# Kernel tuning notes

Measured on AMD Instinct MI355X. Metric: run time of the kernel, lower is better.

The kernel has to match this reference:

```python
import jax, jax.numpy as jnp
import numpy as np

B, H, V, A, NANN, DEPTH = 32, 256, 512, 3, 8, 7


def preorder_perm(arity, depth):
    # level-order node index -> pre-order position permutation for a full arity-ary tree
    starts = np.cumsum([0] + [arity ** l for l in range(depth + 1)])
    order = []
    def rec(l, p):
        order.append(int(starts[l] + p))
        if l < depth:
            for c in range(arity):
                rec(l + 1, p * arity + c)
    rec(0, 0)
    return np.asarray(order, dtype=np.int32)


def setup_inputs() -> dict:
    key = jax.random.key(0)
    ks = jax.random.split(key, 12)
    s = 0.05
    return {
        "root_hiddens": jax.random.normal(ks[0], (B, H), jnp.float32),
        "ann_table": jax.random.normal(ks[1], (NANN, H), jnp.float32),
        "w1": jax.random.normal(ks[2], (2 * H, H), jnp.float32) * s,
        "b1": jnp.zeros((2 * H,), jnp.float32),
        "w2": jax.random.normal(ks[3], (V, 2 * H), jnp.float32) * s,
        "b2": jnp.zeros((V,), jnp.float32),
        "gru_w_ih": jax.random.normal(ks[4], (A, 3 * H, H), jnp.float32) * s,
        "gru_w_hh": jax.random.normal(ks[5], (A, 3 * H, H), jnp.float32) * s,
        "gru_b_ih": jnp.zeros((A, 3 * H), jnp.float32),
        "gru_b_hh": jnp.zeros((A, 3 * H), jnp.float32),
        "ann_ids": jax.random.randint(ks[6], (B,), 0, NANN, jnp.int32),
        "depth": DEPTH,
    }


def _forward(root_hiddens, ann_table, w1, b1, w2, b2,
             gru_w_ih, gru_w_hh, gru_b_ih, gru_b_hh, ann_ids, depth):
    b, h = root_hiddens.shape
    arity = gru_w_ih.shape[0]
    x = ann_table[ann_ids]                                   # [B,H] annotation embedding (GRU input at every node)
    # input-side gates are constant across the whole tree: precompute once
    gx = jnp.einsum('bh,agh->bag', x, gru_w_ih) + gru_b_ih   # [B,A,3H]
    xr, xz, xn = jnp.split(gx, 3, axis=-1)                   # each [B,A,H]

    hid = root_hiddens[:, None, :]                           # [B,1,H]
    levels = [hid]
    for _ in range(depth):
        gh = jnp.einsum('bnh,agh->bnag', hid, gru_w_hh) + gru_b_hh  # [B,n,A,3H]
        hr, hz, hn = jnp.split(gh, 3, axis=-1)
        r = jax.nn.sigmoid(xr[:, None] + hr)
        z = jax.nn.sigmoid(xz[:, None] + hz)
        n = jnp.tanh(xn[:, None] + r * hn)
        new_h = (1.0 - z) * n + z * hid[:, :, None, :]       # [B,n,A,H]
        hid = new_h.reshape(b, -1, h)                        # child c of node p -> p*A+c
        levels.append(hid)

    all_h = jnp.concatenate(levels, axis=1)                  # [B,N,H] level-order
    mid = jax.nn.sigmoid(jnp.einsum('bnh,oh->bno', all_h, w1) + b1)
    prod = jnp.einsum('bno,vo->bnv', mid, w2) + b2           # [B,N,V]
    perm = jnp.asarray(preorder_perm(arity, depth))
    return jnp.transpose(prod[:, perm, :], (1, 0, 2))        # [N,B,V] (seq-first, like pad_sequence)


def reference(root_hiddens, ann_table, w1, b1, w2, b2,
              gru_w_ih, gru_w_hh, gru_b_ih, gru_b_hh, ann_ids, depth):
    return _forward(root_hiddens, ann_table, w1, b1, w2, b2,
                    gru_w_ih, gru_w_hh, gru_b_ih, gru_b_hh, ann_ids, depth)
```

## Files before the change

### kernel.cpp

```cpp
#include <hip/hip_runtime.h>
#include <hip/hip_bf16.h>
#include <stdint.h>
#include <stddef.h>

#define NB 32
#define NH 256
#define NMID 512
#define NV 512
#define NA 3
#define NDEPTH 7
#define NNODES 3280
#define NG 2304
#define MROWS (NNODES * NB)
#define HM 64

typedef __attribute__((ext_vector_type(8))) short bf16x8;
typedef __attribute__((ext_vector_type(4))) float f32x4;

__device__ __forceinline__ unsigned short f2bf(float x) {
    union { float f; unsigned u; } v; v.f = x;
    unsigned r = v.u + 0x7fffu + ((v.u >> 16) & 1u);
    return (unsigned short)(r >> 16);
}
__device__ __forceinline__ unsigned cvt_pk_bf16(float a, float b) {
    unsigned r;
    asm("v_cvt_pk_bf16_f32 %0, %1, %2" : "=v"(r) : "v"(a), "v"(b));
    return r;
}
__device__ __forceinline__ float bf2f(unsigned short u) {
    union { unsigned u; float f; } v; v.u = ((unsigned)u) << 16;
    return v.f;
}
__device__ __forceinline__ float sigm(float x) { return 1.0f / (1.0f + __expf(-x)); }
__device__ __forceinline__ float tanh_(float x) {
    x = fminf(fmaxf(x, -15.0f), 15.0f);
    float e = __expf(2.0f * x);
    return (e - 1.0f) / (e + 1.0f);
}
__device__ __forceinline__ f32x4 splat4(float s) { f32x4 v = {s, s, s, s}; return v; }

__device__ __forceinline__ int preorder_pos(int n) {
    int start = 0, cnt = 1, l = 0;
    while (n >= start + cnt) { start += cnt; cnt *= 3; l++; }
    int p = n - start;
    int pw = 1;
    for (int j = 0; j < l - 1; j++) pw *= 3;
    int pos = 0;
    for (int k = 1; k <= l; k++) {
        int d = (p / pw) % 3;
        int e = NDEPTH - k + 1;
        int p3 = 1; for (int j = 0; j < e; j++) p3 *= 3;
        pos += 1 + d * ((p3 - 1) / 2);
        pw /= 3;
    }
    return pos;
}

__global__ void prep_all(const float* __restrict__ root, const float* __restrict__ ann_table,
                         const int* __restrict__ ann_ids,
                         const float* __restrict__ w_ih, const float* __restrict__ b_ih,
                         const float* __restrict__ whh_f, const float* __restrict__ w1_f,
                         const float* __restrict__ w2_f,
                         unsigned short* __restrict__ whh_b, unsigned short* __restrict__ w1_b,
                         unsigned short* __restrict__ w2_b,
                         float* __restrict__ gx_t, int* __restrict__ posmap,
                         unsigned short* __restrict__ hid_b) {
    int gtid = blockIdx.x * blockDim.x + threadIdx.x;
    int nth = gridDim.x * blockDim.x;
    const int n_whh = NG * NH, n_w1 = NMID * NH, n_w2 = NV * NMID;
    const int total = n_whh + n_w1 + n_w2;
    for (int i = gtid; i < total; i += nth) {
        if (i < n_whh) whh_b[i] = f2bf(whh_f[i]);
        else if (i < n_whh + n_w1) w1_b[i - n_whh] = f2bf(w1_f[i - n_whh]);
        else w2_b[i - n_whh - n_w1] = f2bf(w2_f[i - n_whh - n_w1]);
    }
    if (gtid < NB * NH) hid_b[gtid] = f2bf(root[gtid]);
    if (gtid < NNODES) posmap[gtid] = preorder_pos(gtid);
    int lane = threadIdx.x & 63;
    int gw = gtid >> 6;
    int nw = nth >> 6;
    for (int e = gw; e < NB * NG; e += nw) {
        int b = e / NG;
        int col = e - b * NG;
        const float* xr = ann_table + (size_t)ann_ids[b] * NH;
        const float* wr = w_ih + (size_t)col * NH;
        float4 xv = *(const float4*)(xr + lane * 4);
        float4 wv = *(const float4*)(wr + lane * 4);
        float s = xv.x * wv.x + xv.y * wv.y + xv.z * wv.z + xv.w * wv.w;
        #pragma unroll
        for (int off = 32; off; off >>= 1) s += __shfl_down(s, off);
        if (lane == 0) gx_t[(size_t)col * NB + b] = s + b_ih[col];
    }
}

template<int NPB>
__global__ __launch_bounds__(512, 2)
void gru_level(const unsigned short* __restrict__ hid_b_in,
               unsigned short* __restrict__ hid_b_out,
               const unsigned short* __restrict__ whh_b,
               const float* __restrict__ b_hh, const float* __restrict__ gx_t,
               int start, int child_start, int cnt) {
    constexpr int M = 32 * NPB;
    __shared__ char a_s[M * 512];

    int tid = threadIdx.x;
    int lane = tid & 63;
    int wv = tid >> 6;
    int lr = lane & 15;
    int kg = (lane >> 4) * 8;
    int rbase = (lane >> 4) * 4;
    int nrel0 = blockIdx.x * NPB;
    size_t prow0 = (size_t)(start + nrel0) * NB;

    for (int c = tid; c < M * 32; c += 512) {
        int row = c >> 5;
        int coloff = (c & 31) * 8;
        bf16x8 v = *(const bf16x8*)(hid_b_in + (prow0 + row) * NH + coloff);
        *(bf16x8*)(a_s + ((row * 512 + coloff * 2) ^ ((row & 15) << 4))) = v;
    }
    __syncthreads();

    int Gb = (blockIdx.y * 8 + wv) * 16;
    int a = Gb >> 8;
    int colh = (Gb & 255) + lr;
    int gcol = a * 768 + colh;
    const unsigned short* bptr = whh_b + (size_t)(a * 512 + Gb + lr) * NH + kg;

    float bhr = b_hh[gcol], bhz = b_hh[gcol + 256], bhn = b_hh[gcol + 512];

    f32x4 acc[3][2 * NPB];
    #pragma unroll
    for (int g = 0; g < 2; ++g) {
        f32x4 gr = *(const f32x4*)(gx_t + (size_t)gcol * NB + g * 16 + rbase);
        f32x4 gz = *(const f32x4*)(gx_t + (size_t)(gcol + 256) * NB + g * 16 + rbase);
        #pragma unroll
        for (int mi = g; mi < 2 * NPB; mi += 2) {
            acc[0][mi] = gr + splat4(bhr);
            acc[1][mi] = gz + splat4(bhz);
            acc[2][mi] = splat4(bhn);
        }
    }

    bf16x8 bcur[3];
    #pragma unroll
    for (int t = 0; t < 3; ++t) bcur[t] = *(const bf16x8*)(bptr + t * 256 * NH);
    #pragma unroll
    for (int k0 = 0; k0 < NH; k0 += 32) {
        bf16x8 bnxt[3];
        if (k0 + 32 < NH) {
            #pragma unroll
            for (int t = 0; t < 3; ++t) bnxt[t] = *(const bf16x8*)(bptr + t * 256 * NH + k0 + 32);
        }
        bf16x8 af[2 * NPB];
        #pragma unroll
        for (int mi = 0; mi < 2 * NPB; ++mi) {
            int row = mi * 16 + lr;
            af[mi] = *(const bf16x8*)(a_s + ((row * 512 + (k0 + kg) * 2) ^ ((row & 15) << 4)));
        }
        #pragma unroll
        for (int t = 0; t < 3; ++t)
            #pragma unroll
            for (int mi = 0; mi < 2 * NPB; ++mi)
                acc[t][mi] = __builtin_amdgcn_mfma_f32_16x16x32_bf16(af[mi], bcur[t], acc[t][mi], 0, 0, 0);
        if (k0 + 32 < NH) {
            #pragma unroll
            for (int t = 0; t < 3; ++t) bcur[t] = bnxt[t];
        }
    }

    f32x4 gxn[2];
    #pragma unroll
    for (int g = 0; g < 2; ++g)
        gxn[g] = *(const f32x4*)(gx_t + (size_t)(gcol + 512) * NB + g * 16 + rbase);
    #pragma unroll
    for (int mi = 0; mi < 2 * NPB; ++mi) {
        int ns = (mi * 16 + rbase) >> 5;
        if (nrel0 + ns >= cnt) continue;
        size_t crow = ((size_t)(child_start + (nrel0 + ns) * 3 + a)) * NB;
        float hnew[4];
        #pragma unroll
        for (int j = 0; j < 4; ++j) {
            int row = mi * 16 + rbase + j;
            float r = sigm(acc[0][mi][j]);
            float z = sigm(acc[1][mi][j]);
            float nn = tanh_(gxn[mi & 1][j] + r * acc[2][mi][j]);
            unsigned short hpu = *(const unsigned short*)(a_s + ((row * 512 + colh * 2) ^ ((row & 15) << 4)));
            hnew[j] = (1.0f - z) * nn + z * bf2f(hpu);
        }
        unsigned u01 = cvt_pk_bf16(hnew[0], hnew[1]);
        unsigned u23 = cvt_pk_bf16(hnew[2], hnew[3]);
        int b0 = (mi * 16 + rbase) & 31;
        hid_b_out[(crow + b0 + 0) * NH + colh] = (unsigned short)u01;
        hid_b_out[(crow + b0 + 1) * NH + colh] = (unsigned short)(u01 >> 16);
        hid_b_out[(crow + b0 + 2) * NH + colh] = (unsigned short)u23;
        hid_b_out[(crow + b0 + 3) * NH + colh] = (unsigned short)(u23 >> 16);
    }
}

__global__ __launch_bounds__(512, 4)
void head_fused(const unsigned short* __restrict__ hid_b,
                const unsigned short* __restrict__ w1_b, const float* __restrict__ b1,
                const unsigned short* __restrict__ w2_b, const float* __restrict__ b2,
                const int* __restrict__ posmap, float* __restrict__ out) {
    __shared__ char smem[HM * NMID * 2];

    int tid = threadIdx.x;
    int lane = tid & 63;
    int wv = tid >> 6;
    int mbase = blockIdx.x * HM;
    int lr = lane & 15;
    int kg = (lane >> 4) * 8;
    int rbase = (lane >> 4) * 4;
    int n0w = wv * 64;

    for (int c = tid; c < HM * 32; c += 512) {
        int row = c >> 5;
        int coloff = (c & 31) * 8;
        bf16x8 v = *(const bf16x8*)(hid_b + ((size_t)(mbase + row)) * NH + coloff);
        *(bf16x8*)(smem + ((row * 512 + coloff * 2) ^ ((row & 15) << 4))) = v;
    }
    __syncthreads();

    f32x4 acc[4][4];
    #pragma unroll
    for (int mi = 0; mi < 4; ++mi)
        #pragma unroll
        for (int ni = 0; ni < 4; ++ni) acc[mi][ni] = (f32x4){0.f, 0.f, 0.f, 0.f};

    {
        const unsigned short* bbase = w1_b + ((size_t)(n0w + lr)) * NH + kg;
        bf16x8 bcur[4];
        #pragma unroll
        for (int ni = 0; ni < 4; ++ni) bcur[ni] = *(const bf16x8*)(bbase + ni * 16 * NH);
        #pragma unroll
        for (int k0 = 0; k0 < NH; k0 += 32) {
            bf16x8 bnxt[4];
            if (k0 + 32 < NH) {
                #pragma unroll
                for (int ni = 0; ni < 4; ++ni) bnxt[ni] = *(const bf16x8*)(bbase + ni * 16 * NH + k0 + 32);
            }
            bf16x8 af[4];
            #pragma unroll
            for (int mi = 0; mi < 4; ++mi) {
                int row = mi * 16 + lr;
                af[mi] = *(const bf16x8*)(smem + ((row * 512 + (k0 + kg) * 2) ^ ((row & 15) << 4)));
            }
            #pragma unroll
            for (int mi = 0; mi < 4; ++mi)
                #pragma unroll
                for (int ni = 0; ni < 4; ++ni)
                    acc[mi][ni] = __builtin_amdgcn_mfma_f32_16x16x32_bf16(af[mi], bcur[ni], acc[mi][ni], 0, 0, 0);
            if (k0 + 32 < NH) {
                #pragma unroll
                for (int ni = 0; ni < 4; ++ni) bcur[ni] = bnxt[ni];
            }
        }
    }
    __syncthreads();

    #pragma unroll
    for (int mi = 0; mi < 4; ++mi)
        #pragma unroll
        for (int ni = 0; ni < 4; ++ni) {
            int col = n0w + ni * 16 + lr;
            float bv = b1[col];
            float v0 = sigm(acc[mi][ni][0] + bv);
            float v1 = sigm(acc[mi][ni][1] + bv);
            float v2 = sigm(acc[mi][ni][2] + bv);
            float v3 = sigm(acc[mi][ni][3] + bv);
            unsigned u01 = cvt_pk_bf16(v0, v1);
            unsigned u23 = cvt_pk_bf16(v2, v3);
            int r0 = mi * 16 + rbase;
            *(unsigned short*)(smem + (((r0 + 0) * 1024 + col * 2) ^ (((r0 + 0) & 15) << 4))) = (unsigned short)u01;
            *(unsigned short*)(smem + (((r0 + 1) * 1024 + col * 2) ^ (((r0 + 1) & 15) << 4))) = (unsigned short)(u01 >> 16);
            *(unsigned short*)(smem + (((r0 + 2) * 1024 + col * 2) ^ (((r0 + 2) & 15) << 4))) = (unsigned short)u23;
            *(unsigned short*)(smem + (((r0 + 3) * 1024 + col * 2) ^ (((r0 + 3) & 15) << 4))) = (unsigned short)(u23 >> 16);
        }
    __syncthreads();

    #pragma unroll
    for (int mi = 0; mi < 4; ++mi)
        #pragma unroll
        for (int ni = 0; ni < 4; ++ni) acc[mi][ni] = (f32x4){0.f, 0.f, 0.f, 0.f};
    {
        const unsigned short* bbase = w2_b + ((size_t)(n0w + lr)) * NMID + kg;
        bf16x8 bcur[4];
        #pragma unroll
        for (int ni = 0; ni < 4; ++ni) bcur[ni] = *(const bf16x8*)(bbase + ni * 16 * NMID);
        #pragma unroll
        for (int k0 = 0; k0 < NMID; k0 += 32) {
            bf16x8 bnxt[4];
            if (k0 + 32 < NMID) {
                #pragma unroll
                for (int ni = 0; ni < 4; ++ni) bnxt[ni] = *(const bf16x8*)(bbase + ni * 16 * NMID + k0 + 32);
            }
            bf16x8 af[4];
            #pragma unroll
            for (int mi = 0; mi < 4; ++mi) {
                int row = mi * 16 + lr;
                af[mi] = *(const bf16x8*)(smem + ((row * 1024 + (k0 + kg) * 2) ^ ((row & 15) << 4)));
            }
            #pragma unroll
            for (int mi = 0; mi < 4; ++mi)
                #pragma unroll
                for (int ni = 0; ni < 4; ++ni)
                    acc[mi][ni] = __builtin_amdgcn_mfma_f32_16x16x32_bf16(af[mi], bcur[ni], acc[mi][ni], 0, 0, 0);
            if (k0 + 32 < NMID) {
                #pragma unroll
                for (int ni = 0; ni < 4; ++ni) bcur[ni] = bnxt[ni];
            }
        }
    }
    __syncthreads();

    float bv4[4];
    #pragma unroll
    for (int ni = 0; ni < 4; ++ni) bv4[ni] = b2[n0w + ni * 16 + lr];
    #pragma unroll
    for (int h = 0; h < 2; ++h) {
        #pragma unroll
        for (int mm = 0; mm < 2; ++mm) {
            int mi = h * 2 + mm;
            #pragma unroll
            for (int ni = 0; ni < 4; ++ni) {
                int col = n0w + ni * 16 + lr;
                #pragma unroll
                for (int j = 0; j < 4; ++j) {
                    int rl = mm * 16 + rbase + j;
                    int byteoff = (rl * 2048 + col * 4) ^ ((rl & 7) << 4);
                    *(float*)(smem + byteoff) = acc[mi][ni][j] + bv4[ni];
                }
            }
        }
        __syncthreads();
        int pos = posmap[blockIdx.x * 2 + h];
        float* obase = out + (size_t)pos * NB * NV;
        #pragma unroll
        for (int i = 0; i < 8; ++i) {
            int f = tid + i * 512;
            int rl = f >> 7;
            int cq = f & 127;
            int byteoff = (rl * 2048 + cq * 16) ^ ((rl & 7) << 4);
            f32x4 v = *(const f32x4*)(smem + byteoff);
            *(f32x4*)(obase + (size_t)rl * NV + cq * 4) = v;
        }
        if (h == 0) __syncthreads();
    }
}

extern "C" void kernel_launch(void* const* d_in, const int* in_sizes, int n_in,
                              void* d_out, int out_size, void* d_ws, size_t ws_size,
                              hipStream_t stream) {
    const float* root      = (const float*)d_in[0];
    const float* ann_table = (const float*)d_in[1];
    const float* w1        = (const float*)d_in[2];
    const float* b1        = (const float*)d_in[3];
    const float* w2        = (const float*)d_in[4];
    const float* b2        = (const float*)d_in[5];
    const float* w_ih      = (const float*)d_in[6];
    const float* w_hh      = (const float*)d_in[7];
    const float* b_ih      = (const float*)d_in[8];
    const float* b_hh      = (const float*)d_in[9];
    const int*   ann_ids   = (const int*)d_in[10];

    uint8_t* ws = (uint8_t*)d_ws;
    unsigned short* whh_b = (unsigned short*)ws; ws += (size_t)NG * NH * 2;
    unsigned short* w1_b  = (unsigned short*)ws; ws += (size_t)NMID * NH * 2;
    unsigned short* w2_b  = (unsigned short*)ws; ws += (size_t)NV * NMID * 2;
    float* gx_t           = (float*)ws;          ws += (size_t)NB * NG * 4;
    int* posmap           = (int*)ws;            ws += (size_t)NNODES * 4;
    unsigned short* hid_b = (unsigned short*)ws; ws += (size_t)NNODES * NB * NH * 2;

    prep_all<<<1024, 256, 0, stream>>>(root, ann_table, ann_ids, w_ih, b_ih,
                                       w_hh, w1, w2, whh_b, w1_b, w2_b,
                                       gx_t, posmap, hid_b);

    int start = 0, cnt = 1;
    for (int l = 0; l < NDEPTH; ++l) {
        int child_start = start + cnt;
        if (cnt >= 243) {
            gru_level<4><<<dim3((cnt + 3) / 4, 6), 512, 0, stream>>>(
                hid_b, hid_b, whh_b, b_hh, gx_t, start, child_start, cnt);
        } else {
            gru_level<1><<<dim3(cnt, 6), 512, 0, stream>>>(
                hid_b, hid_b, whh_b, b_hh, gx_t, start, child_start, cnt);
        }
        start = child_start; cnt *= 3;
    }
    head_fused<<<MROWS / HM, 512, 0, stream>>>(hid_b, w1_b, b1, w2_b, b2, posmap, (float*)d_out);
}
```

Before: 377.6 us.

## Process two row tiles per head block with prefetch, direct stores, and MFMA priority

Measured after the change: 1.001 ms. 2.65x slower.

```diff
diff --git a/kernel.cpp b/kernel.cpp
--- a/kernel.cpp
+++ b/kernel.cpp
@@ -157,11 +157,13 @@
             int row = mi * 16 + lr;
             af[mi] = *(const bf16x8*)(a_s + ((row * 512 + (k0 + kg) * 2) ^ ((row & 15) << 4)));
         }
+        __builtin_amdgcn_s_setprio(1);
         #pragma unroll
         for (int t = 0; t < 3; ++t)
             #pragma unroll
             for (int mi = 0; mi < 2 * NPB; ++mi)
                 acc[t][mi] = __builtin_amdgcn_mfma_f32_16x16x32_bf16(af[mi], bcur[t], acc[t][mi], 0, 0, 0);
+        __builtin_amdgcn_s_setprio(0);
         if (k0 + 32 < NH) {
             #pragma unroll
             for (int t = 0; t < 3; ++t) bcur[t] = bnxt[t];
@@ -207,145 +209,165 @@
     int tid = threadIdx.x;
     int lane = tid & 63;
     int wv = tid >> 6;
-    int mbase = blockIdx.x * HM;
+    int mbase0 = blockIdx.x * 2 * HM;
     int lr = lane & 15;
     int kg = (lane >> 4) * 8;
     int rbase = (lane >> 4) * 4;
     int n0w = wv * 64;
 
-    for (int c = tid; c < HM * 32; c += 512) {
+    const unsigned short* bbase1 = w1_b + ((size_t)(n0w + lr)) * NH + kg;
+    const unsigned short* bbase2 = w2_b + ((size_t)(n0w + lr)) * NMID + kg;
+    float bv1 = b1[n0w + (lane & 15)];
+
+    #pragma unroll
+    for (int i = 0; i < 4; ++i) {
+        int c = tid + i * 512;
         int row = c >> 5;
         int coloff = (c & 31) * 8;
-        bf16x8 v = *(const bf16x8*)(hid_b + ((size_t)(mbase + row)) * NH + coloff);
+        bf16x8 v = *(const bf16x8*)(hid_b + ((size_t)(mbase0 + row)) * NH + coloff);
         *(bf16x8*)(smem + ((row * 512 + coloff * 2) ^ ((row & 15) << 4))) = v;
     }
     __syncthreads();
 
-    f32x4 acc[4][4];
-    #pragma unroll
-    for (int mi = 0; mi < 4; ++mi)
-        #pragma unroll
-        for (int ni = 0; ni < 4; ++ni) acc[mi][ni] = (f32x4){0.f, 0.f, 0.f, 0.f};
-
-    {
-        const unsigned short* bbase = w1_b + ((size_t)(n0w + lr)) * NH + kg;
-        bf16x8 bcur[4];
-        #pragma unroll
-        for (int ni = 0; ni < 4; ++ni) bcur[ni] = *(const bf16x8*)(bbase + ni * 16 * NH);
-        #pragma unroll
-        for (int k0 = 0; k0 < NH; k0 += 32) {
-            bf16x8 bnxt[4];
-            if (k0 + 32 < NH) {
+    bf16x8 areg[4];
+
+    for (int t = 0; t < 2; ++t) {
+        int mbase = mbase0 + t * HM;
+
+        f32x4 acc[4][4];
+        #pragma unroll
+        for (int mi = 0; mi < 4; ++mi)
+            #pragma unroll
+            for (int ni = 0; ni < 4; ++ni) acc[mi][ni] = (f32x4){0.f, 0.f, 0.f, 0.f};
+
+        {
+            bf16x8 bcur[4];
+            #pragma unroll
+            for (int ni = 0; ni < 4; ++ni) bcur[ni] = *(const bf16x8*)(bbase1 + ni * 16 * NH);
+            #pragma unroll
+            for (int k0 = 0; k0 < NH; k0 += 32) {
+                bf16x8 bnxt[4];
+                if (k0 + 32 < NH) {
+                    #pragma unroll
+                    for (int ni = 0; ni < 4; ++ni) bnxt[ni] = *(const bf16x8*)(bbase1 + ni * 16 * NH + k0 + 32);
+                }
+                bf16x8 af[4];
                 #pragma unroll
-                for (int ni = 0; ni < 4; ++ni) bnxt[ni] = *(const bf16x8*)(bbase + ni * 16 * NH + k0 + 32);
-            }
-            bf16x8 af[4];
-            #pragma unroll
-            for (int mi = 0; mi < 4; ++mi) {
-                int row = mi * 16 + lr;
-                af[mi] = *(const bf16x8*)(smem + ((row * 512 + (k0 + kg) * 2) ^ ((row & 15) << 4)));
-            }
-            #pragma unroll
-            for (int mi = 0; mi < 4; ++mi)
+                for (int mi = 0; mi < 4; ++mi) {
+                    int row = mi * 16 + lr;
+                    af[mi] = *(const bf16x8*)(smem + ((row * 512 + (k0 + kg) * 2) ^ ((row & 15) << 4)));
+                }
+                __builtin_amdgcn_s_setprio(1);
+                #pragma unroll
+                for (int mi = 0; mi < 4; ++mi)
+                    #pragma unroll
+                    for (int ni = 0; ni < 4; ++ni)
+                        acc[mi][ni] = __builtin_amdgcn_mfma_f32_16x16x32_bf16(af[mi], bcur[ni], acc[mi][ni], 0, 0, 0);
+                __builtin_amdgcn_s_setprio(0);
+                if (k0 + 32 < NH) {
+                    #pragma unroll
+                    for (int ni = 0; ni < 4; ++ni) bcur[ni] = bnxt[ni];
+                }
+            }
+        }
+
+        if (t == 0) {
+            #pragma unroll
+            for (int i = 0; i < 4; ++i) {
+                int c = tid + i * 512;
+                int row = c >> 5;
+                int coloff = (c & 31) * 8;
+                areg[i] = *(const bf16x8*)(hid_b + ((size_t)(mbase0 + HM + row)) * NH + coloff);
+            }
+        }
+        __syncthreads();
+
+        #pragma unroll
+        for (int mi = 0; mi < 4; ++mi)
+            #pragma unroll
+            for (int ni = 0; ni < 4; ++ni) {
+                int col = n0w + ni * 16 + lr;
+                float bv = b1[col];
+                float v0 = sigm(acc[mi][ni][0] + bv);
+                float v1 = sigm(acc[mi][ni][1] + bv);
+                float v2 = sigm(acc[mi][ni][2] + bv);
+                float v3 = sigm(acc[mi][ni][3] + bv);
+                unsigned u01 = cvt_pk_bf16(v0, v1);
+                unsigned u23 = cvt_pk_bf16(v2, v3);
+                int r0 = mi * 16 + rbase;
+                *(unsigned short*)(smem + (((r0 + 0) * 1024 + col * 2) ^ (((r0 + 0) & 15) << 4))) = (unsigned short)u01;
+                *(unsigned short*)(smem + (((r0 + 1) * 1024 + col * 2) ^ (((r0 + 1) & 15) << 4))) = (unsigned short)(u01 >> 16);
+                *(unsigned short*)(smem + (((r0 + 2) * 1024 + col * 2) ^ (((r0 + 2) & 15) << 4))) = (unsigned short)u23;
+                *(unsigned short*)(smem + (((r0 + 3) * 1024 + col * 2) ^ (((r0 + 3) & 15) << 4))) = (unsigned short)(u23 >> 16);
+            }
+        __syncthreads();
+
+        #pragma unroll
+        for (int mi = 0; mi < 4; ++mi)
+            #pragma unroll
+            for (int ni = 0; ni < 4; ++ni) acc[mi][ni] = (f32x4){0.f, 0.f, 0.f, 0.f};
+        {
+            bf16x8 bcur[4];
+            #pragma unroll
+            for (int ni = 0; ni < 4; ++ni) bcur[ni] = *(const bf16x8*)(bbase2 + ni * 16 * NMID);
+            #pragma unroll
+            for (int k0 = 0; k0 < NMID; k0 += 32) {
+                bf16x8 bnxt[4];
+                if (k0 + 32 < NMID) {
+                    #pragma unroll
+                    for (int ni = 0; ni < 4; ++ni) bnxt[ni] = *(const bf16x8*)(bbase2 + ni * 16 * NMID + k0 + 32);
+                }
+                bf16x8 af[4];
+                #pragma unroll
+                for (int mi = 0; mi < 4; ++mi) {
+                    int row = mi * 16 + lr;
+                    af[mi] = *(const bf16x8*)(smem + ((row * 1024 + (k0 + kg) * 2) ^ ((row & 15) << 4)));
+                }
+                __builtin_amdgcn_s_setprio(1);
+                #pragma unroll
+                for (int mi = 0; mi < 4; ++mi)
+                    #pragma unroll
+                    for (int ni = 0; ni < 4; ++ni)
+                        acc[mi][ni] = __builtin_amdgcn_mfma_f32_16x16x32_bf16(af[mi], bcur[ni], acc[mi][ni], 0, 0, 0);
+                __builtin_amdgcn_s_setprio(0);
+                if (k0 + 32 < NMID) {
+                    #pragma unroll
+                    for (int ni = 0; ni < 4; ++ni) bcur[ni] = bnxt[ni];
+                }
+            }
+        }
+        __syncthreads();
+
+        if (t == 0) {
+            #pragma unroll
+            for (int i = 0; i < 4; ++i) {
+                int c = tid + i * 512;
+                int row = c >> 5;
+                int coloff = (c & 31) * 8;
+                *(bf16x8*)(smem + ((row * 512 + coloff * 2) ^ ((row & 15) << 4))) = areg[i];
+            }
+        }
+
+        float bv4[4];
+        #pragma unroll
+        for (int ni = 0; ni < 4; ++ni) bv4[ni] = b2[n0w + ni * 16 + lr];
+        #pragma unroll
+        for (int mi = 0; mi < 4; ++mi) {
+            int row0 = mbase + mi * 16 + rbase;
+            #pragma unroll
+            for (int j = 0; j < 4; ++j) {
+                int row = row0 + j;
+                int b = row & 31;
+                int node = row >> 5;
+                float* orow = out + ((size_t)posmap[node] * NB + b) * NV + n0w + lr;
                 #pragma unroll
                 for (int ni = 0; ni < 4; ++ni)
-                    acc[mi][ni] = __builtin_amdgcn_mfma_f32_16x16x32_bf16(af[mi], bcur[ni], acc[mi][ni], 0, 0, 0);
-            if (k0 + 32 < NH) {
-                #pragma unroll
-                for (int ni = 0; ni < 4; ++ni) bcur[ni] = bnxt[ni];
-            }
-        }
-    }
-    __syncthreads();
-
-    #pragma unroll
-    for (int mi = 0; mi < 4; ++mi)
-        #pragma unroll
-        for (int ni = 0; ni < 4; ++ni) {
-            int col = n0w + ni * 16 + lr;
-            float bv = b1[col];
-            float v0 = sigm(acc[mi][ni][0] + bv);
-            float v1 = sigm(acc[mi][ni][1] + bv);
-            float v2 = sigm(acc[mi][ni][2] + bv);
-            float v3 = sigm(acc[mi][ni][3] + bv);
-            unsigned u01 = cvt_pk_bf16(v0, v1);
-            unsigned u23 = cvt_pk_bf16(v2, v3);
-            int r0 = mi * 16 + rbase;
-            *(unsigned short*)(smem + (((r0 + 0) * 1024 + col * 2) ^ (((r0 + 0) & 15) << 4))) = (unsigned short)u01;
-            *(unsigned short*)(smem + (((r0 + 1) * 1024 + col * 2) ^ (((r0 + 1) & 15) << 4))) = (unsigned short)(u01 >> 16);
-            *(unsigned short*)(smem + (((r0 + 2) * 1024 + col * 2) ^ (((r0 + 2) & 15) << 4))) = (unsigned short)u23;
-            *(unsigned short*)(smem + (((r0 + 3) * 1024 + col * 2) ^ (((r0 + 3) & 15) << 4))) = (unsigned short)(u23 >> 16);
-        }
-    __syncthreads();
-
-    #pragma unroll
-    for (int mi = 0; mi < 4; ++mi)
-        #pragma unroll
-        for (int ni = 0; ni < 4; ++ni) acc[mi][ni] = (f32x4){0.f, 0.f, 0.f, 0.f};
-    {
-        const unsigned short* bbase = w2_b + ((size_t)(n0w + lr)) * NMID + kg;
-        bf16x8 bcur[4];
-        #pragma unroll
-        for (int ni = 0; ni < 4; ++ni) bcur[ni] = *(const bf16x8*)(bbase + ni * 16 * NMID);
-        #pragma unroll
-        for (int k0 = 0; k0 < NMID; k0 += 32) {
-            bf16x8 bnxt[4];
-            if (k0 + 32 < NMID) {
-                #pragma unroll
-                for (int ni = 0; ni < 4; ++ni) bnxt[ni] = *(const bf16x8*)(bbase + ni * 16 * NMID + k0 + 32);
-            }
-            bf16x8 af[4];
-            #pragma unroll
-            for (int mi = 0; mi < 4; ++mi) {
-                int row = mi * 16 + lr;
-                af[mi] = *(const bf16x8*)(smem + ((row * 1024 + (k0 + kg) * 2) ^ ((row & 15) << 4)));
-            }
-            #pragma unroll
-            for (int mi = 0; mi < 4; ++mi)
-                #pragma unroll
-                for (int ni = 0; ni < 4; ++ni)
-                    acc[mi][ni] = __builtin_amdgcn_mfma_f32_16x16x32_bf16(af[mi], bcur[ni], acc[mi][ni], 0, 0, 0);
-            if (k0 + 32 < NMID) {
-                #pragma unroll
-                for (int ni = 0; ni < 4; ++ni) bcur[ni] = bnxt[ni];
-            }
-        }
-    }
-    __syncthreads();
-
-    float bv4[4];
-    #pragma unroll
-    for (int ni = 0; ni < 4; ++ni) bv4[ni] = b2[n0w + ni * 16 + lr];
-    #pragma unroll
-    for (int h = 0; h < 2; ++h) {
-        #pragma unroll
-        for (int mm = 0; mm < 2; ++mm) {
-            int mi = h * 2 + mm;
-            #pragma unroll
-            for (int ni = 0; ni < 4; ++ni) {
-                int col = n0w + ni * 16 + lr;
-                #pragma unroll
-                for (int j = 0; j < 4; ++j) {
-                    int rl = mm * 16 + rbase + j;
-                    int byteoff = (rl * 2048 + col * 4) ^ ((rl & 7) << 4);
-                    *(float*)(smem + byteoff) = acc[mi][ni][j] + bv4[ni];
-                }
-            }
-        }
-        __syncthreads();
-        int pos = posmap[blockIdx.x * 2 + h];
-        float* obase = out + (size_t)pos * NB * NV;
-        #pragma unroll
-        for (int i = 0; i < 8; ++i) {
-            int f = tid + i * 512;
-            int rl = f >> 7;
-            int cq = f & 127;
-            int byteoff = (rl * 2048 + cq * 16) ^ ((rl & 7) << 4);
-            f32x4 v = *(const f32x4*)(smem + byteoff);
-            *(f32x4*)(obase + (size_t)rl * NV + cq * 4) = v;
-        }
-        if (h == 0) __syncthreads();
-    }
+                    orow[ni * 16] = acc[mi][ni][j] + bv4[ni];
+            }
+        }
+        if (t == 0) __syncthreads();
+    }
+    (void)bv1;
 }
 
 extern "C" void kernel_launch(void* const* d_in, const int* in_sizes, int n_in,
@@ -378,8 +400,11 @@
     int start = 0, cnt = 1;
     for (int l = 0; l < NDEPTH; ++l) {
         int child_start = start + cnt;
-        if (cnt >= 243) {
+        if (cnt >= 729) {
             gru_level<4><<<dim3((cnt + 3) / 4, 6), 512, 0, stream>>>(
+                hid_b, hid_b, whh_b, b_hh, gx_t, start, child_start, cnt);
+        } else if (cnt >= 128) {
+            gru_level<2><<<dim3((cnt + 1) / 2, 6), 512, 0, stream>>>(
                 hid_b, hid_b, whh_b, b_hh, gx_t, start, child_start, cnt);
         } else {
             gru_level<1><<<dim3(cnt, 6), 512, 0, stream>>>(
@@ -387,5 +412,5 @@
         }
         start = child_start; cnt *= 3;
     }
-    head_fused<<<MROWS / HM, 512, 0, stream>>>(hid_b, w1_b, b1, w2_b, b2, posmap, (float*)d_out);
-}
+    head_fused<<<MROWS / (2 * HM), 512, 0, stream>>>(hid_b, w1_b, b1, w2_b, b2, posmap, (float*)d_out);
+}
```
